# Kernel tuning notes

Hardware: AMD Instinct MI355X
Metric: run time of the kernel (lower is better)

The kernel has to match this reference:

```python
import jax, jax.numpy as jnp
import numpy as np

DIM = 768
HEADS = 16
DIM_HEAD = DIM // HEADS
SCALE = DIM_HEAD ** -0.5


def setup_inputs() -> dict:
    key = jax.random.key(0)
    k1, k2, k3, k4 = jax.random.split(key, 4)
    B, N = 8, 1024
    x = jax.random.normal(k1, (B, N, DIM), dtype=jnp.float32)
    # nn.Linear(dim, 3*dim, bias=False): stored so that qkv = x @ Wqkv
    Wqkv = jax.random.normal(k2, (DIM, 3 * DIM), dtype=jnp.float32) * (DIM ** -0.5)
    Wo = jax.random.normal(k3, (DIM, DIM), dtype=jnp.float32) * (DIM ** -0.5)
    bo = jax.random.normal(k4, (DIM,), dtype=jnp.float32) * 0.01
    return {"x": x, "Wqkv": Wqkv, "Wo": Wo, "bo": bo}


def reference(x, Wqkv, Wo, bo):
    B, N, _ = x.shape
    qkv = x @ Wqkv                                   # [B, N, 3*dim]
    # Faithful to torch: qkv.view(3, B, h, N, dim_head) — raw memory reshape
    qkv = jnp.reshape(qkv, (3, B, HEADS, N, DIM_HEAD))
    q, k, v = qkv[0], qkv[1], qkv[2]                 # each [B, h, N, dh]
    attn = jnp.einsum('bhnd,bhmd->bhnm', q, k) * SCALE   # [B, h, N, N]
    weight = jax.nn.softmax(attn, axis=-1)
    context = jnp.einsum('bhnm,bhmd->bhnd', weight, v)   # [B, h, N, dh]
    # Faithful to torch: context.view(B, -1, dim) — raw memory reshape
    concat = jnp.reshape(context, (B, N, DIM))
    return concat @ Wo + bo                          # dropout is identity at eval
```

## Files before the change

### kernel.cpp

```cpp
#include <hip/hip_runtime.h>
#include <hip/hip_bf16.h>

typedef __bf16 bf16x8 __attribute__((ext_vector_type(8)));
typedef __bf16 bf16x4 __attribute__((ext_vector_type(4)));
typedef float  f32x4  __attribute__((ext_vector_type(4)));

#define C2LOG 0.20823509f

__device__ __forceinline__ void gload_lds16(const __bf16* g, __bf16* l) {
    __builtin_amdgcn_global_load_lds(
        (const __attribute__((address_space(1))) void*)g,
        (__attribute__((address_space(3))) void*)l,
        16, 0, 0);
}

__global__ __launch_bounds__(256)
void prepass_kernel(const float* __restrict__ x, const float* __restrict__ Wqkv,
                    const float* __restrict__ Wo, __bf16* __restrict__ Xbf,
                    __bf16* __restrict__ WqkvT, __bf16* __restrict__ WoT) {
    __shared__ float tile[32][33];
    const int bx = blockIdx.x, t = threadIdx.x;
    if (bx < 6144) {
        const int i = (bx * 256 + t) * 4;
        float4 v = *(const float4*)&x[i];
        bf16x4 o;
        o[0] = (__bf16)v.x; o[1] = (__bf16)v.y; o[2] = (__bf16)v.z; o[3] = (__bf16)v.w;
        *(bf16x4*)&Xbf[i] = o;
        return;
    }
    const float* in; __bf16* out; int R, C, bxx;
    if (bx < 6144 + 1728) { bxx = bx - 6144; in = Wqkv; out = WqkvT; R = 768; C = 2304;
        const int c0 = (bxx % 72) * 32, r0 = (bxx / 72) * 32;
        const int tx = t & 31, ty = t >> 5;
#pragma unroll
        for (int i = 0; i < 4; ++i)
            tile[ty + i * 8][tx] = in[(size_t)(r0 + ty + i * 8) * C + c0 + tx];
        __syncthreads();
#pragma unroll
        for (int i = 0; i < 4; ++i)
            out[(size_t)(c0 + ty + i * 8) * R + r0 + tx] = (__bf16)tile[tx][ty + i * 8];
    } else { bxx = bx - 6144 - 1728; in = Wo; out = WoT; R = 768; C = 768;
        const int c0 = (bxx % 24) * 32, r0 = (bxx / 24) * 32;
        const int tx = t & 31, ty = t >> 5;
#pragma unroll
        for (int i = 0; i < 4; ++i)
            tile[ty + i * 8][tx] = in[(size_t)(r0 + ty + i * 8) * C + c0 + tx];
        __syncthreads();
#pragma unroll
        for (int i = 0; i < 4; ++i)
            out[(size_t)(c0 + ty + i * 8) * R + r0 + tx] = (__bf16)tile[tx][ty + i * 8];
    }
}

__global__ __launch_bounds__(256, 3)
void gemm_bt_kernel(const __bf16* __restrict__ A, const __bf16* __restrict__ B,
                    __bf16* __restrict__ C, int M, int N, int K) {
    __shared__ __bf16 sA[128 * 32];
    __shared__ __bf16 sB[128 * 32];

    const int m0 = blockIdx.y * 128;
    const int n0 = blockIdx.x * 128;
    const int t = threadIdx.x;
    const int w = t >> 6, lane = t & 63;
    const int quad = lane >> 4, l15 = lane & 15;
    const int wm = w >> 1, wn = w & 1;

    f32x4 acc[4][4] = {};

    for (int k0 = 0; k0 < K; k0 += 32) {
#pragma unroll
        for (int half = 0; half < 2; ++half) {
            const int row = half * 64 + w * 16 + (lane >> 2);
            const int kk = k0 + (lane & 3) * 8;
            gload_lds16(A + (size_t)(m0 + row) * K + kk, &sA[half * 2048 + w * 512]);
            gload_lds16(B + (size_t)(n0 + row) * K + kk, &sB[half * 2048 + w * 512]);
        }
        __syncthreads();

        bf16x8 aF[4], bF[4];
#pragma unroll
        for (int mt = 0; mt < 4; ++mt)
            aF[mt] = *(const bf16x8*)&sA[(wm * 64 + mt * 16 + l15) * 32 + quad * 8];
#pragma unroll
        for (int nt = 0; nt < 4; ++nt)
            bF[nt] = *(const bf16x8*)&sB[(wn * 64 + nt * 16 + l15) * 32 + quad * 8];
#pragma unroll
        for (int mt = 0; mt < 4; ++mt)
#pragma unroll
            for (int nt = 0; nt < 4; ++nt)
                acc[mt][nt] = __builtin_amdgcn_mfma_f32_16x16x32_bf16(aF[mt], bF[nt], acc[mt][nt], 0, 0, 0);
        __syncthreads();
    }

#pragma unroll
    for (int nt = 0; nt < 4; ++nt) {
        const int col = n0 + wn * 64 + nt * 16 + l15;
#pragma unroll
        for (int mt = 0; mt < 4; ++mt)
#pragma unroll
            for (int r = 0; r < 4; ++r) {
                const int row = m0 + wm * 64 + mt * 16 + quad * 4 + r;
                C[(size_t)row * N + col] = (__bf16)acc[mt][nt][r];
            }
    }
}

__global__ __launch_bounds__(256, 4)
void gemm_bt64_kernel(const __bf16* __restrict__ A, const __bf16* __restrict__ B,
                      float* __restrict__ C, const float* __restrict__ bias,
                      int M, int N, int K) {
    __shared__ __bf16 sA[128 * 32];
    __shared__ __bf16 sB[64 * 32];

    const int m0 = blockIdx.y * 128;
    const int n0 = blockIdx.x * 64;
    const int t = threadIdx.x;
    const int w = t >> 6, lane = t & 63;
    const int quad = lane >> 4, l15 = lane & 15;

    f32x4 acc[2][4] = {};

    for (int k0 = 0; k0 < K; k0 += 32) {
        const int kk = k0 + (lane & 3) * 8;
#pragma unroll
        for (int p = 0; p < 2; ++p) {
            const int row = w * 32 + p * 16 + (lane >> 2);
            gload_lds16(A + (size_t)(m0 + row) * K + kk, &sA[w * 1024 + p * 512]);
        }
        {
            const int row = w * 16 + (lane >> 2);
            gload_lds16(B + (size_t)(n0 + row) * K + kk, &sB[w * 512]);
        }
        __syncthreads();

        bf16x8 aF[2], bF[4];
#pragma unroll
        for (int mt = 0; mt < 2; ++mt)
            aF[mt] = *(const bf16x8*)&sA[(w * 32 + mt * 16 + l15) * 32 + quad * 8];
#pragma unroll
        for (int nt = 0; nt < 4; ++nt)
            bF[nt] = *(const bf16x8*)&sB[(nt * 16 + l15) * 32 + quad * 8];
#pragma unroll
        for (int mt = 0; mt < 2; ++mt)
#pragma unroll
            for (int nt = 0; nt < 4; ++nt)
                acc[mt][nt] = __builtin_amdgcn_mfma_f32_16x16x32_bf16(aF[mt], bF[nt], acc[mt][nt], 0, 0, 0);
        __syncthreads();
    }

#pragma unroll
    for (int nt = 0; nt < 4; ++nt) {
        const int col = n0 + nt * 16 + l15;
        const float bv = bias[col];
#pragma unroll
        for (int mt = 0; mt < 2; ++mt)
#pragma unroll
            for (int r = 0; r < 4; ++r) {
                const int row = m0 + w * 32 + mt * 16 + quad * 4 + r;
                C[(size_t)row * N + col] = acc[mt][nt][r] + bv;
            }
    }
}

#define VT_STRIDE 132
#define P_STRIDE  132

__global__ __launch_bounds__(512, 4)
void attn_kernel(const __bf16* __restrict__ Y1, __bf16* __restrict__ Ctx) {
    __shared__ __bf16 Kl[128 * 64];
    __shared__ __bf16 Vt[48 * VT_STRIDE];
    __shared__ __bf16 Pl[128 * P_STRIDE];

    const int bx = blockIdx.x;
    const int bh = bx & 127, qt = bx >> 7;
    const int t = threadIdx.x, w = t >> 6, lane = t & 63;
    const int quad = lane >> 4, l15 = lane & 15;

    const size_t qBase = (size_t)bh * 49152;
    const size_t kBase = 6291456 + qBase;
    const size_t vBase = 12582912 + qBase;

    bf16x8 qf0, qf1;
    {
        const int row = qt * 128 + w * 16 + l15;
        qf0 = *(const bf16x8*)(Y1 + qBase + (size_t)row * 48 + quad * 8);
        if (quad < 2)
            qf1 = *(const bf16x8*)(Y1 + qBase + (size_t)row * 48 + 32 + quad * 8);
        else
            qf1 = bf16x8{};
    }

    const int kr0 = t >> 3, kd0 = t & 7;
    const int kr1 = (t + 512) >> 3, kd1 = (t + 512) & 7;
    int vkp[3], vdb[3], vkk[3];
#pragma unroll
    for (int c = 0; c < 3; ++c) {
        const int u = t + c * 512;
        vkp[c] = u & 127;
        vdb[c] = (u >> 7) * 4;
        vkk[c] = (vkp[c] >> 3) + ((vkp[c] & 7) << 4);
    }

    bf16x8 kreg0 = *(const bf16x8*)(Y1 + kBase + (size_t)kr0 * 48 + kd0 * 8);
    bf16x8 kreg1 = *(const bf16x8*)(Y1 + kBase + (size_t)kr1 * 48 + kd1 * 8);
    bf16x4 vreg[3];
#pragma unroll
    for (int c = 0; c < 3; ++c)
        vreg[c] = *(const bf16x4*)(Y1 + vBase + (size_t)vkk[c] * 48 + vdb[c]);

    f32x4 o[3] = {};
    float l_lane[4] = {0.f, 0.f, 0.f, 0.f};

    for (int it = 0; it < 8; ++it) {
        __syncthreads();

        *(bf16x8*)&Kl[kr0 * 64 + ((kd0 ^ (kr0 & 7)) << 3)] = kreg0;
        *(bf16x8*)&Kl[kr1 * 64 + ((kd1 ^ (kr1 & 7)) << 3)] = kreg1;
#pragma unroll
        for (int c = 0; c < 3; ++c)
#pragma unroll
            for (int j = 0; j < 4; ++j)
                Vt[(vdb[c] + j) * VT_STRIDE + vkp[c]] = vreg[c][j];

        if (it < 7) {
            const int kv1 = (it + 1) * 128;
            kreg0 = *(const bf16x8*)(Y1 + kBase + (size_t)(kv1 + kr0) * 48 + kd0 * 8);
            kreg1 = *(const bf16x8*)(Y1 + kBase + (size_t)(kv1 + kr1) * 48 + kd1 * 8);
#pragma unroll
            for (int c = 0; c < 3; ++c)
                vreg[c] = *(const bf16x4*)(Y1 + vBase + (size_t)(kv1 + vkk[c]) * 48 + vdb[c]);
        }

        __syncthreads();

        f32x4 s[8];
#pragma unroll
        for (int nt = 0; nt < 8; ++nt) {
            const int krow = nt * 16 + l15;
            const int base = krow * 64;
            bf16x8 kf0 = *(const bf16x8*)&Kl[base + ((quad ^ (krow & 7)) << 3)];
            bf16x8 kf1 = *(const bf16x8*)&Kl[base + (((4 + quad) ^ (krow & 7)) << 3)];
            f32x4 z = {};
            z = __builtin_amdgcn_mfma_f32_16x16x32_bf16(qf0, kf0, z, 0, 0, 0);
            s[nt] = __builtin_amdgcn_mfma_f32_16x16x32_bf16(qf1, kf1, z, 0, 0, 0);
        }

#pragma unroll
        for (int r = 0; r < 4; ++r) {
            bf16x8 pk;
            float ls = 0.f;
#pragma unroll
            for (int nt = 0; nt < 8; ++nt) {
                float p = __builtin_amdgcn_exp2f(s[nt][r] * C2LOG);
                ls += p;
                pk[nt] = (__bf16)p;
            }
            l_lane[r] += ls;
            *(bf16x8*)&Pl[(w * 16 + quad * 4 + r) * P_STRIDE + l15 * 8] = pk;
        }

        bf16x8 pa[4];
#pragma unroll
        for (int ks = 0; ks < 4; ++ks)
            pa[ks] = *(const bf16x8*)&Pl[(w * 16 + l15) * P_STRIDE + ks * 32 + quad * 8];
#pragma unroll
        for (int nt = 0; nt < 3; ++nt) {
#pragma unroll
            for (int ks = 0; ks < 4; ++ks) {
                bf16x8 vb = *(const bf16x8*)&Vt[(nt * 16 + l15) * VT_STRIDE + ks * 32 + quad * 8];
                o[nt] = __builtin_amdgcn_mfma_f32_16x16x32_bf16(pa[ks], vb, o[nt], 0, 0, 0);
            }
        }
    }

    float inv[4];
#pragma unroll
    for (int r = 0; r < 4; ++r) {
        float ls = l_lane[r];
#pragma unroll
        for (int off = 1; off < 16; off <<= 1)
            ls += __shfl_xor(ls, off);
        inv[r] = __builtin_amdgcn_rcpf(ls);
    }

    __syncthreads();
    __bf16* Ob = Vt;
#pragma unroll
    for (int nt = 0; nt < 3; ++nt) {
        const int d = nt * 16 + l15;
#pragma unroll
        for (int r = 0; r < 4; ++r)
            Ob[(w * 16 + quad * 4 + r) * 48 + d] = (__bf16)(o[nt][r] * inv[r]);
    }
    __syncthreads();
    __bf16* dst = Ctx + qBase + (size_t)qt * 128 * 48;
    *(bf16x8*)(dst + t * 8) = *(const bf16x8*)&Ob[t * 8];
    if (t < 256)
        *(bf16x8*)(dst + (t + 512) * 8) = *(const bf16x8*)&Ob[(t + 512) * 8];
}

extern "C" void kernel_launch(void* const* d_in, const int* in_sizes, int n_in,
                              void* d_out, int out_size, void* d_ws, size_t ws_size,
                              hipStream_t stream) {
    const float* x    = (const float*)d_in[0];
    const float* Wqkv = (const float*)d_in[1];
    const float* Wo   = (const float*)d_in[2];
    const float* bo   = (const float*)d_in[3];
    float* out = (float*)d_out;

    char* ws = (char*)d_ws;
    __bf16* Xbf    = (__bf16*)(ws + 0);
    __bf16* WqkvT  = (__bf16*)(ws + 12582912);
    __bf16* WoT    = (__bf16*)(ws + 16121856);
    __bf16* Y1     = (__bf16*)(ws + 17301504);
    __bf16* Ctx    = (__bf16*)(ws + 55050240);

    prepass_kernel<<<8448, 256, 0, stream>>>(x, Wqkv, Wo, Xbf, WqkvT, WoT);

    gemm_bt_kernel<<<dim3(18, 64), 256, 0, stream>>>(Xbf, WqkvT, Y1, 8192, 2304, 768);

    attn_kernel<<<1024, 512, 0, stream>>>(Y1, Ctx);

    gemm_bt64_kernel<<<dim3(12, 64), 256, 0, stream>>>(Ctx, WoT, out, bo, 8192, 768, 768);
}
```

Before: 205.2 us.

## Double GEMM K-tile to 64 with XOR-swizzled LDS layout

Both bf16 GEMM kernels now stage 64-wide K slices per iteration instead of 32, halving the number of barrier pairs per K loop. The LDS layout is XOR-swizzled on 16-byte chunks, and the fragment reads apply the same swizzle, to avoid bank conflicts at the wider 128-byte row stride. LDS use per block doubles, which may reduce how many blocks fit on a CU.

```diff
diff --git a/kernel.cpp b/kernel.cpp
--- a/kernel.cpp
+++ b/kernel.cpp
@@ -55,8 +55,8 @@
 __global__ __launch_bounds__(256, 3)
 void gemm_bt_kernel(const __bf16* __restrict__ A, const __bf16* __restrict__ B,
                     __bf16* __restrict__ C, int M, int N, int K) {
-    __shared__ __bf16 sA[128 * 32];
-    __shared__ __bf16 sB[128 * 32];
+    __shared__ __bf16 sA[128 * 64];
+    __shared__ __bf16 sB[128 * 64];
 
     const int m0 = blockIdx.y * 128;
     const int n0 = blockIdx.x * 128;
@@ -65,30 +65,41 @@
     const int quad = lane >> 4, l15 = lane & 15;
     const int wm = w >> 1, wn = w & 1;
 
+    int aRow[4], aKc[4];
+#pragma unroll
+    for (int b = 0; b < 4; ++b) {
+        const int L = b * 256 + t;
+        aRow[b] = L >> 3;
+        aKc[b] = (L & 7) ^ (aRow[b] & 7);
+    }
+
     f32x4 acc[4][4] = {};
 
-    for (int k0 = 0; k0 < K; k0 += 32) {
-#pragma unroll
-        for (int half = 0; half < 2; ++half) {
-            const int row = half * 64 + w * 16 + (lane >> 2);
-            const int kk = k0 + (lane & 3) * 8;
-            gload_lds16(A + (size_t)(m0 + row) * K + kk, &sA[half * 2048 + w * 512]);
-            gload_lds16(B + (size_t)(n0 + row) * K + kk, &sB[half * 2048 + w * 512]);
-        }
-        __syncthreads();
-
-        bf16x8 aF[4], bF[4];
-#pragma unroll
-        for (int mt = 0; mt < 4; ++mt)
-            aF[mt] = *(const bf16x8*)&sA[(wm * 64 + mt * 16 + l15) * 32 + quad * 8];
-#pragma unroll
-        for (int nt = 0; nt < 4; ++nt)
-            bF[nt] = *(const bf16x8*)&sB[(wn * 64 + nt * 16 + l15) * 32 + quad * 8];
-#pragma unroll
-        for (int mt = 0; mt < 4; ++mt)
+    for (int k0 = 0; k0 < K; k0 += 64) {
+#pragma unroll
+        for (int b = 0; b < 4; ++b) {
+            const int ldsOff = (b * 256 + w * 64) * 8;
+            gload_lds16(A + (size_t)(m0 + aRow[b]) * K + k0 + aKc[b] * 8, &sA[ldsOff]);
+            gload_lds16(B + (size_t)(n0 + aRow[b]) * K + k0 + aKc[b] * 8, &sB[ldsOff]);
+        }
+        __syncthreads();
+
+#pragma unroll
+        for (int ks = 0; ks < 2; ++ks) {
+            bf16x8 aF[4], bF[4];
+            const int slot = ((ks * 4 + quad) ^ (l15 & 7)) * 8;
+#pragma unroll
+            for (int mt = 0; mt < 4; ++mt)
+                aF[mt] = *(const bf16x8*)&sA[(wm * 64 + mt * 16 + l15) * 64 + slot];
 #pragma unroll
             for (int nt = 0; nt < 4; ++nt)
-                acc[mt][nt] = __builtin_amdgcn_mfma_f32_16x16x32_bf16(aF[mt], bF[nt], acc[mt][nt], 0, 0, 0);
+                bF[nt] = *(const bf16x8*)&sB[(wn * 64 + nt * 16 + l15) * 64 + slot];
+#pragma unroll
+            for (int mt = 0; mt < 4; ++mt)
+#pragma unroll
+                for (int nt = 0; nt < 4; ++nt)
+                    acc[mt][nt] = __builtin_amdgcn_mfma_f32_16x16x32_bf16(aF[mt], bF[nt], acc[mt][nt], 0, 0, 0);
+        }
         __syncthreads();
     }
 
@@ -109,8 +120,8 @@
 void gemm_bt64_kernel(const __bf16* __restrict__ A, const __bf16* __restrict__ B,
                       float* __restrict__ C, const float* __restrict__ bias,
                       int M, int N, int K) {
-    __shared__ __bf16 sA[128 * 32];
-    __shared__ __bf16 sB[64 * 32];
+    __shared__ __bf16 sA[128 * 64];
+    __shared__ __bf16 sB[64 * 64];
 
     const int m0 = blockIdx.y * 128;
     const int n0 = blockIdx.x * 64;
@@ -118,33 +129,43 @@
     const int w = t >> 6, lane = t & 63;
     const int quad = lane >> 4, l15 = lane & 15;
 
+    int sRow[4], sKc[4];
+#pragma unroll
+    for (int b = 0; b < 4; ++b) {
+        const int L = b * 256 + t;
+        sRow[b] = L >> 3;
+        sKc[b] = (L & 7) ^ (sRow[b] & 7);
+    }
+
     f32x4 acc[2][4] = {};
 
-    for (int k0 = 0; k0 < K; k0 += 32) {
-        const int kk = k0 + (lane & 3) * 8;
-#pragma unroll
-        for (int p = 0; p < 2; ++p) {
-            const int row = w * 32 + p * 16 + (lane >> 2);
-            gload_lds16(A + (size_t)(m0 + row) * K + kk, &sA[w * 1024 + p * 512]);
-        }
-        {
-            const int row = w * 16 + (lane >> 2);
-            gload_lds16(B + (size_t)(n0 + row) * K + kk, &sB[w * 512]);
-        }
-        __syncthreads();
-
-        bf16x8 aF[2], bF[4];
-#pragma unroll
-        for (int mt = 0; mt < 2; ++mt)
-            aF[mt] = *(const bf16x8*)&sA[(w * 32 + mt * 16 + l15) * 32 + quad * 8];
-#pragma unroll
-        for (int nt = 0; nt < 4; ++nt)
-            bF[nt] = *(const bf16x8*)&sB[(nt * 16 + l15) * 32 + quad * 8];
-#pragma unroll
-        for (int mt = 0; mt < 2; ++mt)
+    for (int k0 = 0; k0 < K; k0 += 64) {
+#pragma unroll
+        for (int b = 0; b < 4; ++b)
+            gload_lds16(A + (size_t)(m0 + sRow[b]) * K + k0 + sKc[b] * 8,
+                        &sA[(b * 256 + w * 64) * 8]);
+#pragma unroll
+        for (int b = 0; b < 2; ++b)
+            gload_lds16(B + (size_t)(n0 + sRow[b]) * K + k0 + sKc[b] * 8,
+                        &sB[(b * 256 + w * 64) * 8]);
+        __syncthreads();
+
+#pragma unroll
+        for (int ks = 0; ks < 2; ++ks) {
+            bf16x8 aF[2], bF[4];
+            const int slot = ((ks * 4 + quad) ^ (l15 & 7)) * 8;
+#pragma unroll
+            for (int mt = 0; mt < 2; ++mt)
+                aF[mt] = *(const bf16x8*)&sA[(w * 32 + mt * 16 + l15) * 64 + slot];
 #pragma unroll
             for (int nt = 0; nt < 4; ++nt)
-                acc[mt][nt] = __builtin_amdgcn_mfma_f32_16x16x32_bf16(aF[mt], bF[nt], acc[mt][nt], 0, 0, 0);
+                bF[nt] = *(const bf16x8*)&sB[(nt * 16 + l15) * 64 + slot];
+#pragma unroll
+            for (int mt = 0; mt < 2; ++mt)
+#pragma unroll
+                for (int nt = 0; nt < 4; ++nt)
+                    acc[mt][nt] = __builtin_amdgcn_mfma_f32_16x16x32_bf16(aF[mt], bF[nt], acc[mt][nt], 0, 0, 0);
+        }
         __syncthreads();
     }
 
```

Result: faster. 199.8 us (-2.6%).
